# Kernel tuning notes

Hardware: AMD Instinct MI355X
Metric: run time of the kernel (lower is better)

Reference implementation:

```python
import jax, jax.numpy as jnp
import numpy as np

OUT_H, OUT_W = 7, 7
SPATIAL_SCALE = 0.25
SAMPLE_NUM = 2
N_ORI = 8
CLOCKWISE = False


def setup_inputs() -> dict:
    key = jax.random.key(0)
    k1, k2, k3, k4, k5 = jax.random.split(key, 5)
    B, Ct, H, W = 2, 256, 256, 256
    n_rois = 512
    features = jax.random.normal(k1, (B, Ct, H, W), dtype=jnp.float32)
    img = H / SPATIAL_SCALE  # image-space extent = 1024
    batch_ind = jax.random.randint(k2, (n_rois,), 0, B).astype(jnp.float32)
    cxy = jax.random.uniform(k3, (n_rois, 2), minval=0.0, maxval=img, dtype=jnp.float32)
    wh = jax.random.uniform(k4, (n_rois, 2), minval=16.0, maxval=img / 4.0, dtype=jnp.float32)
    ang = jax.random.uniform(k5, (n_rois, 1), minval=-np.pi, maxval=np.pi, dtype=jnp.float32)
    rois = jnp.concatenate([batch_ind[:, None], cxy, wh, ang], axis=1)  # (n, 6)
    return {"features": features, "rois": rois}


def _bilinear(feat, y, x):
    # feat: (Ct, H, W); y, x: (P,) -> (Ct, P). Matches mmcv bilinear_interpolate.
    Ct, H, W = feat.shape
    valid = (y >= -1.0) & (y <= H) & (x >= -1.0) & (x <= W)
    y = jnp.maximum(y, 0.0)
    x = jnp.maximum(x, 0.0)
    y0 = jnp.minimum(jnp.floor(y).astype(jnp.int32), H - 1)
    x0 = jnp.minimum(jnp.floor(x).astype(jnp.int32), W - 1)
    y1 = jnp.minimum(y0 + 1, H - 1)
    x1 = jnp.minimum(x0 + 1, W - 1)
    ly = jnp.where(y0 >= H - 1, 0.0, y - y0.astype(y.dtype))
    lx = jnp.where(x0 >= W - 1, 0.0, x - x0.astype(x.dtype))
    hy, hx = 1.0 - ly, 1.0 - lx
    v = ((hy * hx) * feat[:, y0, x0] + (hy * lx) * feat[:, y0, x1]
         + (ly * hx) * feat[:, y1, x0] + (ly * lx) * feat[:, y1, x1])
    return v * valid.astype(feat.dtype)[None, :]


def _per_roi(features, roi):
    B, Ctot, H, W = features.shape
    C = Ctot // N_ORI
    b = roi[0].astype(jnp.int32)
    cx = roi[1] * SPATIAL_SCALE  # roi_center_w
    cy = roi[2] * SPATIAL_SCALE  # roi_center_h
    rw = jnp.maximum(roi[3] * SPATIAL_SCALE, 1.0)
    rh = jnp.maximum(roi[4] * SPATIAL_SCALE, 1.0)
    theta = roi[5]
    bin_h = rh / OUT_H
    bin_w = rw / OUT_W
    # orientation channel alignment (uses un-flipped theta)
    ind_f = theta * N_ORI / (2.0 * jnp.pi)
    ind = jnp.floor(ind_f).astype(jnp.int32)
    l_var = ind_f - ind.astype(theta.dtype)
    r_var = 1.0 - l_var
    ind = jnp.mod(ind, N_ORI)
    th = -theta if CLOCKWISE else theta
    cos_t, sin_t = jnp.cos(th), jnp.sin(th)
    gh = gw = SAMPLE_NUM
    # sample grid in roi-centered coords: yy (OUT_H, gh), xx (OUT_W, gw)
    yy = -rh / 2.0 + (jnp.arange(OUT_H)[:, None] + (jnp.arange(gh) + 0.5) / gh) * bin_h
    xx = -rw / 2.0 + (jnp.arange(OUT_W)[:, None] + (jnp.arange(gw) + 0.5) / gw) * bin_w
    Y = yy[:, None, :, None]  # (OUT_H,1,gh,1)
    X = xx[None, :, None, :]  # (1,OUT_W,1,gw)
    y = (Y * cos_t - X * sin_t + cy).reshape(-1)  # (P,)
    x = (Y * sin_t + X * cos_t + cx).reshape(-1)
    feat = features[b]  # (Ctot, H, W)
    vals = _bilinear(feat, y, x).reshape(C, N_ORI, OUT_H, OUT_W, gh, gw)
    o = jnp.arange(N_ORI)
    idx = jnp.mod(o - ind, N_ORI)
    idx_p = jnp.mod(idx + 1, N_ORI)
    mixed = r_var * vals[:, idx] + l_var * vals[:, idx_p]  # cyclic orientation shift + interp
    out = mixed.mean(axis=(-1, -2))  # average over bin sample grid
    return out.reshape(Ctot, OUT_H, OUT_W)


def reference(features, rois):
    return jax.vmap(lambda r: _per_roi(features, r))(rois)  # (n, Ctot, OUT_H, OUT_W)
```

## Files before the change

### kernel.cpp

```cpp
#include <hip/hip_runtime.h>
#include <hip/hip_fp16.h>
#include <math.h>

#define HH 256
#define WW 256
#define CTOT 256
#define HW (HH * WW)
#define NBIN 49

typedef __attribute__((ext_vector_type(8))) _Float16 half8;
typedef __attribute__((ext_vector_type(4))) float fvec4;

__global__ __launch_bounds__(256) void convert_kernel_v2(
    const float* __restrict__ feats, half8* __restrict__ wsf, int total4 )
{
    const int g = blockIdx.x * 256 + threadIdx.x;
    if (g >= total4) return;
    const int pix = (g & 16383) << 2;
    const int bc  = g >> 14;
    const float* src = feats + ((size_t)bc * 8) * HW + pix;
    fvec4 v[8];
    #pragma unroll
    for (int o = 0; o < 8; ++o)
        v[o] = __builtin_nontemporal_load((const fvec4*)(src + (size_t)o * HW));
    half8* dst = wsf + (size_t)bc * HW + pix;
    #pragma unroll
    for (int j = 0; j < 4; ++j) {
        half8 h;
        h[0] = (_Float16)v[0][j]; h[1] = (_Float16)v[1][j];
        h[2] = (_Float16)v[2][j]; h[3] = (_Float16)v[3][j];
        h[4] = (_Float16)v[4][j]; h[5] = (_Float16)v[5][j];
        h[6] = (_Float16)v[6][j]; h[7] = (_Float16)v[7][j];
        dst[j] = h;
    }
}

__global__ __launch_bounds__(256) void riroi_pool_f16_v3(
    const half8* __restrict__ wsf,
    const float* __restrict__ rois,
    float* __restrict__ out,
    int per_cg4)
{
    const int h = blockIdx.x * 256 + threadIdx.x;
    if (h >= per_cg4) return;
    const int cg  = blockIdx.y;
    const int s   = h & 3;
    const int t   = h >> 2;
    const int n   = t / NBIN;
    const int bin = t - n * NBIN;
    const int ph  = bin / 7;
    const int pw  = bin - ph * 7;

    const float* r = rois + n * 6;
    const int   b     = (int)r[0];
    const float cx    = r[1] * 0.25f;
    const float cy    = r[2] * 0.25f;
    const float rwv   = fmaxf(r[3] * 0.25f, 1.0f);
    const float rhv   = fmaxf(r[4] * 0.25f, 1.0f);
    const float theta = r[5];
    const float bin_h = rhv * (1.0f / 7.0f);
    const float bin_w = rwv * (1.0f / 7.0f);

    const float ind_f = (theta * 8.0f) / 6.28318530717958647692f;
    const int   ind0  = (int)floorf(ind_f);
    const float l_var = ind_f - (float)ind0;
    const float r_var = 1.0f - l_var;
    const int   ind   = ((ind0 % 8) + 8) % 8;
    const float cos_t = cosf(theta);
    const float sin_t = sinf(theta);

    const int gy = s >> 1, gx = s & 1;
    const float yy = -rhv * 0.5f + ((float)ph + ((float)gy + 0.5f) * 0.5f) * bin_h;
    const float xx = -rwv * 0.5f + ((float)pw + ((float)gx + 0.5f) * 0.5f) * bin_w;
    const float y  = yy * cos_t - xx * sin_t + cy;
    const float x  = yy * sin_t + xx * cos_t + cx;
    const float valid =
        (y >= -1.0f && y <= 256.0f && x >= -1.0f && x <= 256.0f) ? 1.0f : 0.0f;
    const float yc = fmaxf(y, 0.0f);
    const float xc = fmaxf(x, 0.0f);
    const int y0 = min((int)floorf(yc), HH - 1);
    const int x0 = min((int)floorf(xc), WW - 1);
    const int y1 = min(y0 + 1, HH - 1);
    const float ly = (y0 >= HH - 1) ? 0.0f : (yc - (float)y0);
    const float lx = (x0 >= WW - 1) ? 0.0f : (xc - (float)x0);
    const float hy = 1.0f - ly, hx = 1.0f - lx;
    const float sc = 0.25f * valid;
    const int   xb = min(x0, WW - 2);
    const float cw0 = (x0 < WW - 1) ? hx : 0.0f;
    const float cw1 = (x0 < WW - 1) ? lx : hx;
    const float w00 = hy * sc * cw0;
    const float w01 = hy * sc * cw1;
    const float w10 = ly * sc * cw0;
    const float w11 = ly * sc * cw1;
    const int off0 = (y0 << 8) + xb;
    const int off1 = (y1 << 8) + xb;

    const half8* base = wsf + (size_t)(b * 32 + cg) * HW;

    const half8 q0 = base[off0];
    const half8 q1 = base[off0 + 1];
    const half8 q2 = base[off1];
    const half8 q3 = base[off1 + 1];

    float acc[8];
    #pragma unroll
    for (int o = 0; o < 8; ++o)
        acc[o] = w00 * (float)q0[o] + w01 * (float)q1[o]
               + w10 * (float)q2[o] + w11 * (float)q3[o];

    #pragma unroll
    for (int o = 0; o < 8; ++o) {
        acc[o] += __shfl_xor(acc[o], 1, 64);
        acc[o] += __shfl_xor(acc[o], 2, 64);
    }

    float* obase = out + ((size_t)n * CTOT + (size_t)(cg * 8)) * NBIN + bin;
    switch (s) {
    case 0:
        __builtin_nontemporal_store(r_var * acc[0] + l_var * acc[1], obase + (((0 + ind) & 7) * NBIN));
        __builtin_nontemporal_store(r_var * acc[1] + l_var * acc[2], obase + (((1 + ind) & 7) * NBIN));
        break;
    case 1:
        __builtin_nontemporal_store(r_var * acc[2] + l_var * acc[3], obase + (((2 + ind) & 7) * NBIN));
        __builtin_nontemporal_store(r_var * acc[3] + l_var * acc[4], obase + (((3 + ind) & 7) * NBIN));
        break;
    case 2:
        __builtin_nontemporal_store(r_var * acc[4] + l_var * acc[5], obase + (((4 + ind) & 7) * NBIN));
        __builtin_nontemporal_store(r_var * acc[5] + l_var * acc[6], obase + (((5 + ind) & 7) * NBIN));
        break;
    default:
        __builtin_nontemporal_store(r_var * acc[6] + l_var * acc[7], obase + (((6 + ind) & 7) * NBIN));
        __builtin_nontemporal_store(r_var * acc[7] + l_var * acc[0], obase + (((7 + ind) & 7) * NBIN));
        break;
    }
}

__global__ __launch_bounds__(256) void riroi_rotated_fallback(
    const float* __restrict__ feats, const float* __restrict__ rois,
    float* __restrict__ out, int total)
{
    const int g = blockIdx.x * 256 + threadIdx.x;
    if (g >= total) return;
    const int wpr = 32 * NBIN;
    const int n   = g / wpr;
    const int rem = g - n * wpr;
    const int cg  = rem / NBIN;
    const int bin = rem - cg * NBIN;
    const int ph  = bin / 7;
    const int pw  = bin - ph * 7;
    const float* r = rois + n * 6;
    const int   b     = (int)r[0];
    const float cx    = r[1] * 0.25f;
    const float cy    = r[2] * 0.25f;
    const float rwv   = fmaxf(r[3] * 0.25f, 1.0f);
    const float rhv   = fmaxf(r[4] * 0.25f, 1.0f);
    const float theta = r[5];
    const float bin_h = rhv * (1.0f / 7.0f);
    const float bin_w = rwv * (1.0f / 7.0f);
    const float ind_f = (theta * 8.0f) / 6.28318530717958647692f;
    const int   ind0  = (int)floorf(ind_f);
    const float l_var = ind_f - (float)ind0;
    const float r_var = 1.0f - l_var;
    const int   ind   = ((ind0 % 8) + 8) % 8;
    const float cos_t = cosf(theta);
    const float sin_t = sinf(theta);
    int   off0[4], off1[4];
    float rw0[4], rw1[4], cw0[4], cw1[4];
    #pragma unroll
    for (int s = 0; s < 4; ++s) {
        const int gy = s >> 1, gx = s & 1;
        const float yy = -rhv * 0.5f + ((float)ph + ((float)gy + 0.5f) * 0.5f) * bin_h;
        const float xx = -rwv * 0.5f + ((float)pw + ((float)gx + 0.5f) * 0.5f) * bin_w;
        const float y  = yy * cos_t - xx * sin_t + cy;
        const float x  = yy * sin_t + xx * cos_t + cx;
        const float valid =
            (y >= -1.0f && y <= 256.0f && x >= -1.0f && x <= 256.0f) ? 1.0f : 0.0f;
        const float yc = fmaxf(y, 0.0f);
        const float xc = fmaxf(x, 0.0f);
        const int y0 = min((int)floorf(yc), HH - 1);
        const int x0 = min((int)floorf(xc), WW - 1);
        const int y1 = min(y0 + 1, HH - 1);
        const float ly = (y0 >= HH - 1) ? 0.0f : (yc - (float)y0);
        const float lx = (x0 >= WW - 1) ? 0.0f : (xc - (float)x0);
        const float hy = 1.0f - ly, hx = 1.0f - lx;
        const float sc = 0.25f * valid;
        const int   xb = min(x0, WW - 2);
        cw0[s]  = (x0 < WW - 1) ? hx : 0.0f;
        cw1[s]  = (x0 < WW - 1) ? lx : hx;
        rw0[s]  = hy * sc;
        rw1[s]  = ly * sc;
        off0[s] = (y0 << 8) + xb;
        off1[s] = (y1 << 8) + xb;
    }
    const float* gbase = feats + (size_t)b * (CTOT * HW) + (size_t)(cg * 8) * HW;
    float acc[8];
    #pragma unroll
    for (int o = 0; o < 8; o += 2) {
        const float* pA = gbase + (size_t)o * HW;
        const float* pB = pA + HW;
        float2 q[16];
        #pragma unroll
        for (int s = 0; s < 4; ++s) {
            q[s * 4 + 0] = *(const float2*)(pA + off0[s]);
            q[s * 4 + 1] = *(const float2*)(pA + off1[s]);
            q[s * 4 + 2] = *(const float2*)(pB + off0[s]);
            q[s * 4 + 3] = *(const float2*)(pB + off1[s]);
        }
        float a0 = 0.0f, a1 = 0.0f;
        #pragma unroll
        for (int s = 0; s < 4; ++s) {
            a0 += rw0[s] * (cw0[s] * q[s * 4 + 0].x + cw1[s] * q[s * 4 + 0].y)
                + rw1[s] * (cw0[s] * q[s * 4 + 1].x + cw1[s] * q[s * 4 + 1].y);
            a1 += rw0[s] * (cw0[s] * q[s * 4 + 2].x + cw1[s] * q[s * 4 + 2].y)
                + rw1[s] * (cw0[s] * q[s * 4 + 3].x + cw1[s] * q[s * 4 + 3].y);
        }
        acc[o] = a0; acc[o + 1] = a1;
    }
    float* obase = out + ((size_t)n * CTOT + (size_t)(cg * 8)) * NBIN + bin;
    #pragma unroll
    for (int s = 0; s < 8; ++s) {
        const int o_out = (s + ind) & 7;
        __builtin_nontemporal_store(r_var * acc[s] + l_var * acc[(s + 1) & 7],
                                    obase + o_out * NBIN);
    }
}

extern "C" void kernel_launch(void* const* d_in, const int* in_sizes, int n_in,
                              void* d_out, int out_size, void* d_ws, size_t ws_size,
                              hipStream_t stream) {
    const float* feats = (const float*)d_in[0];
    const float* rois  = (const float*)d_in[1];
    float* out = (float*)d_out;
    const int n_rois = in_sizes[1] / 6;
    const int B      = in_sizes[0] / (CTOT * HW);
    const size_t ws_need = (size_t)B * 32 * HW * sizeof(half8);

    if (ws_size >= ws_need) {
        half8* wsf = (half8*)d_ws;
        const int tc4 = B * 32 * HW / 4;
        convert_kernel_v2<<<(tc4 + 255) / 256, 256, 0, stream>>>(feats, wsf, tc4);
        const int per_cg4 = n_rois * NBIN * 4;
        dim3 grid((per_cg4 + 255) / 256, 32);
        riroi_pool_f16_v3<<<grid, 256, 0, stream>>>(wsf, rois, out, per_cg4);
    } else {
        const int total = n_rois * 32 * NBIN;
        riroi_rotated_fallback<<<(total + 255) / 256, 256, 0, stream>>>(feats, rois, out, total);
    }
}
```

Before: 237.5 us.

## Remap pool blocks so each XCD owns four channel groups; simplify convert

The pool kernel becomes a 1D grid whose block index is decoded so that blocks on the same XCD (block id mod 8) handle the same four channel groups. Blocks that reuse the same slices of the half-precision feature workspace then share an L2. The convert kernel now has each thread handle one pixel with scalar loads instead of four pixels with vector loads. ROI parameters are read as float2 and sin and cos come from a single sincosf call. The risk is narrower loads in the convert pass and an assumed round-robin block-to-XCD dispatch.

```diff
diff --git a/kernel.cpp b/kernel.cpp
--- a/kernel.cpp
+++ b/kernel.cpp
@@ -11,39 +11,37 @@
 typedef __attribute__((ext_vector_type(8))) _Float16 half8;
 typedef __attribute__((ext_vector_type(4))) float fvec4;
 
-__global__ __launch_bounds__(256) void convert_kernel_v2(
-    const float* __restrict__ feats, half8* __restrict__ wsf, int total4 )
+__global__ __launch_bounds__(256) void convert_kernel_v3(
+    const float* __restrict__ feats, half8* __restrict__ wsf, int total )
 {
     const int g = blockIdx.x * 256 + threadIdx.x;
-    if (g >= total4) return;
-    const int pix = (g & 16383) << 2;
-    const int bc  = g >> 14;
+    if (g >= total) return;
+    const int pix = g & (HW - 1);
+    const int bc  = g >> 16;
     const float* src = feats + ((size_t)bc * 8) * HW + pix;
-    fvec4 v[8];
+    half8 h;
     #pragma unroll
     for (int o = 0; o < 8; ++o)
-        v[o] = __builtin_nontemporal_load((const fvec4*)(src + (size_t)o * HW));
-    half8* dst = wsf + (size_t)bc * HW + pix;
-    #pragma unroll
-    for (int j = 0; j < 4; ++j) {
-        half8 h;
-        h[0] = (_Float16)v[0][j]; h[1] = (_Float16)v[1][j];
-        h[2] = (_Float16)v[2][j]; h[3] = (_Float16)v[3][j];
-        h[4] = (_Float16)v[4][j]; h[5] = (_Float16)v[5][j];
-        h[6] = (_Float16)v[6][j]; h[7] = (_Float16)v[7][j];
-        dst[j] = h;
-    }
-}
-
-__global__ __launch_bounds__(256) void riroi_pool_f16_v3(
+        h[o] = (_Float16)__builtin_nontemporal_load(src + (size_t)o * HW);
+    wsf[(size_t)bc * HW + pix] = h;
+}
+
+__global__ __launch_bounds__(256) void riroi_pool_f16_v4(
     const half8* __restrict__ wsf,
     const float* __restrict__ rois,
     float* __restrict__ out,
-    int per_cg4)
+    int per_cg4,
+    int nxblk)
 {
-    const int h = blockIdx.x * 256 + threadIdx.x;
+    const int bid  = blockIdx.x;
+    const int xcd  = bid & 7;
+    const int idx  = bid >> 3;
+    const int cgq  = idx / nxblk;
+    const int xblk = idx - cgq * nxblk;
+    const int cg   = (xcd << 2) + cgq;
+    const int h    = xblk * 256 + threadIdx.x;
     if (h >= per_cg4) return;
-    const int cg  = blockIdx.y;
+
     const int s   = h & 3;
     const int t   = h >> 2;
     const int n   = t / NBIN;
@@ -51,13 +49,15 @@
     const int ph  = bin / 7;
     const int pw  = bin - ph * 7;
 
-    const float* r = rois + n * 6;
-    const int   b     = (int)r[0];
-    const float cx    = r[1] * 0.25f;
-    const float cy    = r[2] * 0.25f;
-    const float rwv   = fmaxf(r[3] * 0.25f, 1.0f);
-    const float rhv   = fmaxf(r[4] * 0.25f, 1.0f);
-    const float theta = r[5];
+    const float2 r01 = *(const float2*)(rois + n * 6);
+    const float2 r23 = *(const float2*)(rois + n * 6 + 2);
+    const float2 r45 = *(const float2*)(rois + n * 6 + 4);
+    const int   b     = (int)r01.x;
+    const float cx    = r01.y * 0.25f;
+    const float cy    = r23.x * 0.25f;
+    const float rwv   = fmaxf(r23.y * 0.25f, 1.0f);
+    const float rhv   = fmaxf(r45.x * 0.25f, 1.0f);
+    const float theta = r45.y;
     const float bin_h = rhv * (1.0f / 7.0f);
     const float bin_w = rwv * (1.0f / 7.0f);
 
@@ -66,8 +66,8 @@
     const float l_var = ind_f - (float)ind0;
     const float r_var = 1.0f - l_var;
     const int   ind   = ((ind0 % 8) + 8) % 8;
-    const float cos_t = cosf(theta);
-    const float sin_t = sinf(theta);
+    float sin_t, cos_t;
+    sincosf(theta, &sin_t, &cos_t);
 
     const int gy = s >> 1, gx = s & 1;
     const float yy = -rhv * 0.5f + ((float)ph + ((float)gy + 0.5f) * 0.5f) * bin_h;
@@ -237,11 +237,12 @@
 
     if (ws_size >= ws_need) {
         half8* wsf = (half8*)d_ws;
-        const int tc4 = B * 32 * HW / 4;
-        convert_kernel_v2<<<(tc4 + 255) / 256, 256, 0, stream>>>(feats, wsf, tc4);
+        const int total = B * 32 * HW;
+        convert_kernel_v3<<<(total + 255) / 256, 256, 0, stream>>>(feats, wsf, total);
         const int per_cg4 = n_rois * NBIN * 4;
-        dim3 grid((per_cg4 + 255) / 256, 32);
-        riroi_pool_f16_v3<<<grid, 256, 0, stream>>>(wsf, rois, out, per_cg4);
+        const int nxblk   = (per_cg4 + 255) / 256;
+        dim3 grid(32 * nxblk);
+        riroi_pool_f16_v4<<<grid, 256, 0, stream>>>(wsf, rois, out, per_cg4, nxblk);
     } else {
         const int total = n_rois * 32 * NBIN;
         riroi_rotated_fallback<<<(total + 255) / 256, 256, 0, stream>>>(feats, rois, out, total);
```

New measurement: 218.0 us, median of 2. 8.2% less time.
